# Performance work log

Measured on AMD Instinct MI355X. Metric: run time of the kernel, lower is better.

## Reference

```python
import jax, jax.numpy as jnp
import numpy as np
import math

K = 3            # max_rings
N_COMP = K + 2   # rings + center + background
RING_S = 0.02
BG_SIGMA = 0.94
CENTER_SIGMA = 0.01
NOISE_CAP = 0.15
COND_DIM, H_DIM = 64, 128
D_IN = COND_DIM + H_DIM


def setup_inputs() -> dict:
    key = jax.random.key(0)
    ks = jax.random.split(key, 12)
    sc = lambda fan_in: 1.0 / np.sqrt(fan_in)
    return {
        "c": jax.random.normal(ks[0], (1, COND_DIM), jnp.float32),
        "h": jax.random.normal(ks[1], (1, H_DIM), jnp.float32),
        # logits MLP: [D_IN, 128, 128, N_COMP]
        "W1": jax.random.normal(ks[2], (D_IN, 128), jnp.float32) * sc(D_IN),
        "b1": jnp.zeros((128,), jnp.float32),
        "W2": jax.random.normal(ks[3], (128, 128), jnp.float32) * sc(128),
        "b2": jnp.zeros((128,), jnp.float32),
        "W3": jax.random.normal(ks[4], (128, N_COMP), jnp.float32) * sc(128),
        "b3": jnp.zeros((N_COMP,), jnp.float32),
        # center_radius head: mus [K,2], Rs [K]
        "W_mu": jax.random.normal(ks[5], (D_IN, K * 2), jnp.float32) * sc(D_IN),
        "b_mu": jnp.zeros((K * 2,), jnp.float32),
        "W_R": jax.random.normal(ks[6], (D_IN, K), jnp.float32) * sc(D_IN),
        "b_R": jnp.ones((K,), jnp.float32) * 0.5,
        "N": 8388608,
    }


def _capped_weights(x, W1, b1, W2, b2, W3, b3):
    z = jax.nn.silu(x @ W1 + b1)
    z = jax.nn.silu(z @ W2 + b2)
    w = jax.nn.softmax(z @ W3 + b3, axis=-1)          # [1, N_COMP]
    w_bg = jnp.minimum(w[..., -1:], NOISE_CAP)
    w_rest = w[..., :-1]
    rest_sum = jnp.maximum(w_rest.sum(-1, keepdims=True), 1e-8)
    w_rest = w_rest * (1.0 - w_bg) / rest_sum
    return jnp.concatenate([w_rest, w_bg], axis=-1) + 1e-8


def reference(c, h, W1, b1, W2, b2, W3, b3, W_mu, b_mu, W_R, b_R, N):
    x = jnp.concatenate([c, h], axis=-1)              # [1, D_IN]
    w = _capped_weights(x, W1, b1, W2, b2, W3, b3)[0]  # [N_COMP]
    mus = (x @ W_mu + b_mu).reshape(K, 2)             # [K, 2]
    Rs = (x @ W_R + b_R)[0]                           # [K]

    key = jax.random.key(42)
    k_cat, k_th, k_r, k_eps = jax.random.split(key, 4)
    idx = jax.random.categorical(k_cat, jnp.log(w), shape=(N,))   # [N]
    jr = jnp.minimum(idx, K - 1)                      # safe ring index

    theta = jax.random.uniform(k_th, (N,), jnp.float32) * (2.0 * math.pi)
    r = Rs[jr] + RING_S * jax.random.normal(k_r, (N,), jnp.float32)
    ring_xy = jnp.stack([r * jnp.cos(theta), r * jnp.sin(theta)], axis=-1) + mus[jr]

    eps = jax.random.normal(k_eps, (N, 2), jnp.float32)
    center_xy = mus[0] + CENTER_SIGMA * eps
    bg_xy = mus[0] + BG_SIGMA * eps

    is_ring = (idx < K)[:, None]
    is_center = (idx == K)[:, None]
    xy = jnp.where(is_ring, ring_xy, jnp.where(is_center, center_xy, bg_xy))
    return xy, idx
```

## Files before the change

kernel.cpp:

```cpp
#include <hip/hip_runtime.h>
#include <math.h>

#define TFROT(v, r) (((v) << (r)) | ((v) >> (32 - (r))))

__device__ __forceinline__ void tf_block(unsigned k0, unsigned k1,
                                         unsigned x0, unsigned x1,
                                         unsigned &o0, unsigned &o1) {
  unsigned ks2 = k0 ^ k1 ^ 0x1BD11BDAu;
  x0 += k0; x1 += k1;
  x0 += x1; x1 = TFROT(x1, 13); x1 ^= x0;
  x0 += x1; x1 = TFROT(x1, 15); x1 ^= x0;
  x0 += x1; x1 = TFROT(x1, 26); x1 ^= x0;
  x0 += x1; x1 = TFROT(x1,  6); x1 ^= x0;
  x0 += k1; x1 += ks2 + 1u;
  x0 += x1; x1 = TFROT(x1, 17); x1 ^= x0;
  x0 += x1; x1 = TFROT(x1, 29); x1 ^= x0;
  x0 += x1; x1 = TFROT(x1, 16); x1 ^= x0;
  x0 += x1; x1 = TFROT(x1, 24); x1 ^= x0;
  x0 += ks2; x1 += k0 + 2u;
  x0 += x1; x1 = TFROT(x1, 13); x1 ^= x0;
  x0 += x1; x1 = TFROT(x1, 15); x1 ^= x0;
  x0 += x1; x1 = TFROT(x1, 26); x1 ^= x0;
  x0 += x1; x1 = TFROT(x1,  6); x1 ^= x0;
  x0 += k0; x1 += k1 + 3u;
  x0 += x1; x1 = TFROT(x1, 17); x1 ^= x0;
  x0 += x1; x1 = TFROT(x1, 29); x1 ^= x0;
  x0 += x1; x1 = TFROT(x1, 16); x1 ^= x0;
  x0 += x1; x1 = TFROT(x1, 24); x1 ^= x0;
  x0 += k1; x1 += ks2 + 4u;
  x0 += x1; x1 = TFROT(x1, 13); x1 ^= x0;
  x0 += x1; x1 = TFROT(x1, 15); x1 ^= x0;
  x0 += x1; x1 = TFROT(x1, 26); x1 ^= x0;
  x0 += x1; x1 = TFROT(x1,  6); x1 ^= x0;
  x0 += ks2; x1 += k0 + 5u;
  o0 = x0; o1 = x1;
}

__device__ __forceinline__ unsigned tf_bits32(unsigned k0, unsigned k1, unsigned i) {
  unsigned o0, o1;
  tf_block(k0, k1, 0u, i, o0, o1);
  return o0 ^ o1;
}

__device__ __forceinline__ float xla_exp_f32(float x) {
#pragma clang fp contract(off)
  const float kHi = 88.3762626647950f;
  const float kLo = -88.3762626647949f;
  const float kLog2e = 1.44269504088896341f;
  const float kC1 = 0.693359375f;
  const float kC2 = -2.12194440e-4f;
  const float p0 = 1.9875691500e-4f, p1 = 1.3981999507e-3f,
              p2 = 8.3334519073e-3f, p3 = 4.1665795894e-2f,
              p4 = 1.6666665459e-1f, p5 = 5.0000001201e-1f;
  float xc = fminf(fmaxf(x, kLo), kHi);
  float t = xc * kLog2e;
  t = t + 0.5f;
  float fx = floorf(t);
  float tmp = kC1 * fx;
  float z = kC2 * fx;
  float xr = xc - tmp;
  xr = xr - z;
  z = xr * xr;
  float y = p0 * xr;  y = y + p1;
  y = y * xr;  y = y + p2;
  y = y * xr;  y = y + p3;
  y = y * xr;  y = y + p4;
  y = y * xr;  y = y + p5;
  y = y * z;   y = y + xr;
  y = 1.0f + y;
  int emm0 = (int)fx;
  emm0 = (emm0 + 0x7f) << 23;
  float two_n = __int_as_float(emm0);
  float res = y * two_n;
  return fmaxf(res, x);
}

__device__ __forceinline__ float xla_log_f32(float x) {
#pragma clang fp contract(off)
  const float kSqrtHf = 0.707106781186547524f;
  const float p0 = 7.0376836292e-2f,  p1 = -1.1514610310e-1f,
              p2 = 1.1676998740e-1f,  p3 = -1.2420140846e-1f,
              p4 = 1.4249322787e-1f,  p5 = -1.6668057665e-1f,
              p6 = 2.0000714765e-1f,  p7 = -2.4999993993e-1f,
              p8 = 3.3333331174e-1f;
  const float q1 = -2.12194440e-4f, q2 = 0.693359375f;
  float t0 = fmaxf(x, __uint_as_float(0x00800000u));
  unsigned ib = __float_as_uint(t0);
  int ei = (int)(ib >> 23) - 0x7f;
  float e = (float)ei;
  e = e + 1.0f;
  t0 = __uint_as_float((ib & 0x807fffffu) | 0x3f000000u);
  bool m = (t0 < kSqrtHf);
  float tmp1 = m ? t0 : 0.0f;
  t0 = t0 - 1.0f;
  e = e - (m ? 1.0f : 0.0f);
  t0 = t0 + tmp1;
  float x2 = t0 * t0;
  float x3 = x2 * t0;
  float y, y1, y2;
  y  = p0 * t0;  y  = y  + p1;
  y1 = p3 * t0;  y1 = y1 + p4;
  y2 = p6 * t0;  y2 = y2 + p7;
  y  = y  * t0;  y  = y  + p2;
  y1 = y1 * t0;  y1 = y1 + p5;
  y2 = y2 * t0;  y2 = y2 + p8;
  y  = y * x3;   y  = y + y1;
  y  = y * x3;   y  = y + y2;
  y  = y * x3;
  y1 = e * q1;
  float tmp2 = x2 * 0.5f;
  y = y + y1;
  t0 = t0 - tmp2;
  y2 = e * q2;
  t0 = t0 + y;
  t0 = t0 + y2;
  return t0;
}

__device__ __forceinline__ float bits_to_f01(unsigned b) {
#pragma clang fp contract(off)
  return __uint_as_float((b >> 9) | 0x3f800000u) - 1.0f;
}

__device__ __forceinline__ float erfinv_f(float x) {
  float t = fmaf(-x, x, 1.0f);
  float w = -__logf(t);
  float p;
  if (w < 5.0f) {
    float v = w - 2.5f;
    p = 2.81022636e-08f;
    p = fmaf(p, v, 3.43273939e-07f);
    p = fmaf(p, v, -3.5233877e-06f);
    p = fmaf(p, v, -4.39150654e-06f);
    p = fmaf(p, v, 0.00021858087f);
    p = fmaf(p, v, -0.00125372503f);
    p = fmaf(p, v, -0.00417768164f);
    p = fmaf(p, v, 0.246640727f);
    p = fmaf(p, v, 1.50140941f);
  } else {
    float v = __fsqrt_rn(w) - 3.0f;
    p = -0.000200214257f;
    p = fmaf(p, v, 0.000100950558f);
    p = fmaf(p, v, 0.00134934322f);
    p = fmaf(p, v, -0.00367342844f);
    p = fmaf(p, v, 0.00573950773f);
    p = fmaf(p, v, -0.0076224613f);
    p = fmaf(p, v, 0.00943887047f);
    p = fmaf(p, v, 1.00167406f);
    p = fmaf(p, v, 2.83297682f);
  }
  return p * x;
}

struct Params {
  double mu[6];
  double Rs[3];
  float logits[5];
  unsigned keys[8];
};

__global__ void prep_kernel(const float* __restrict__ c, const float* __restrict__ h,
                            const float* __restrict__ W1, const float* __restrict__ b1,
                            const float* __restrict__ W2, const float* __restrict__ b2,
                            const float* __restrict__ W3, const float* __restrict__ b3,
                            const float* __restrict__ Wmu, const float* __restrict__ bmu,
                            const float* __restrict__ WR, const float* __restrict__ bR,
                            Params* __restrict__ P) {
#pragma clang fp contract(off)
  __shared__ float xs[192], z1[128], z2[128], z3[5];
  int t = threadIdx.x;
  if (t < 64) xs[t] = c[t];
  else if (t < 192) xs[t] = h[t - 64];
  __syncthreads();
  if (t < 128) {
    float acc = 0.0f;
    for (int k = 0; k < 192; ++k) { float pr = xs[k] * W1[k * 128 + t]; acc = acc + pr; }
    acc = acc + b1[t];
    float ex = xla_exp_f32(-acc);
    float den = 1.0f + ex;
    float sg = 1.0f / den;
    z1[t] = acc * sg;
  }
  __syncthreads();
  if (t < 128) {
    float acc = 0.0f;
    for (int k = 0; k < 128; ++k) { float pr = z1[k] * W2[k * 128 + t]; acc = acc + pr; }
    acc = acc + b2[t];
    float ex = xla_exp_f32(-acc);
    float den = 1.0f + ex;
    float sg = 1.0f / den;
    z2[t] = acc * sg;
  }
  __syncthreads();
  if (t < 5) {
    float acc = 0.0f;
    for (int k = 0; k < 128; ++k) { float pr = z2[k] * W3[k * 5 + t]; acc = acc + pr; }
    z3[t] = acc + b3[t];
  }
  if (t < 6) {
    double acc = 0.0;
    for (int k = 0; k < 192; ++k) acc += (double)xs[k] * (double)Wmu[k * 6 + t];
    P->mu[t] = acc + (double)bmu[t];
  }
  if (t < 3) {
    double acc = 0.0;
    for (int k = 0; k < 192; ++k) acc += (double)xs[k] * (double)WR[k * 3 + t];
    P->Rs[t] = acc + (double)bR[t];
  }
  __syncthreads();
  if (t == 0) {
    float mx = z3[0];
    for (int j = 1; j < 5; ++j) mx = fmaxf(mx, z3[j]);
    float ev[5];
    float ssum = 0.0f;
    for (int j = 0; j < 5; ++j) {
      float d = z3[j] - mx;
      ev[j] = xla_exp_f32(d);
      ssum = ssum + ev[j];
    }
    float w[5];
    for (int j = 0; j < 5; ++j) w[j] = ev[j] / ssum;
    float wbg = fminf(w[4], 0.15f);
    float rsum = 0.0f;
    for (int j = 0; j < 4; ++j) rsum = rsum + w[j];
    float rs = fmaxf(rsum, 1e-8f);
    float om = 1.0f - wbg;
    float wf[5];
    for (int j = 0; j < 4; ++j) {
      float a = w[j] * om;
      float bq = a / rs;
      wf[j] = bq + 1e-8f;
    }
    wf[4] = wbg + 1e-8f;
    for (int j = 0; j < 5; ++j) P->logits[j] = xla_log_f32(wf[j]);
    unsigned a0, a1;
    tf_block(0u, 42u, 0u, 0u, a0, a1); P->keys[0] = a0; P->keys[1] = a1;
    tf_block(0u, 42u, 0u, 1u, a0, a1); P->keys[2] = a0; P->keys[3] = a1;
    tf_block(0u, 42u, 0u, 2u, a0, a1); P->keys[4] = a0; P->keys[5] = a1;
    tf_block(0u, 42u, 0u, 3u, a0, a1); P->keys[6] = a0; P->keys[7] = a1;
  }
}

__global__ void __launch_bounds__(256)
sample_kernel(const Params* __restrict__ P, float* __restrict__ out, int N) {
#pragma clang fp contract(off)
  const float TINYF = __uint_as_float(0x00800000u);
  const float LOF   = __uint_as_float(0xBF7FFFFFu);
  const float TWOPIF = __uint_as_float(0x40C90FDBu);
  const float SQRT2F = 1.4142135623730951f;
  const float MARGIN = 1e-4f;

  float lg[5];
  float muf[6], Rsf[3];
  unsigned ky[8];
#pragma unroll
  for (int j = 0; j < 5; ++j) lg[j] = P->logits[j];
#pragma unroll
  for (int j = 0; j < 6; ++j) muf[j] = (float)P->mu[j];
#pragma unroll
  for (int j = 0; j < 3; ++j) Rsf[j] = (float)P->Rs[j];
#pragma unroll
  for (int j = 0; j < 8; ++j) ky[j] = P->keys[j];

  int T = gridDim.x * blockDim.x;
  for (int s = blockIdx.x * blockDim.x + threadIdx.x; s < N; s += T) {
    unsigned base = 5u * (unsigned)s;
    float uu[5];
    int bi = 0;
    float b1v = -__builtin_inff();
    float b2v = -__builtin_inff();
#pragma unroll
    for (int j = 0; j < 5; ++j) {
      unsigned b = tf_bits32(ky[0], ky[1], base + (unsigned)j);
      float u0 = bits_to_f01(b);
      float u = u0 + TINYF;
      u = fmaxf(TINYF, u);
      uu[j] = u;
      float l1 = __logf(u);
      float l2 = __logf(-l1);
      float sc = lg[j] - l2;
      bool gt = sc > b1v;
      float old1 = b1v;
      b1v = gt ? sc : b1v;
      b2v = gt ? old1 : fmaxf(b2v, sc);
      bi  = gt ? j : bi;
    }
    if (b1v - b2v < MARGIN) {
      int best = 0;
      float bestv = -__builtin_inff();
#pragma unroll
      for (int j = 0; j < 5; ++j) {
        float l1 = xla_log_f32(uu[j]);
        float nl1 = -l1;
        float l2 = xla_log_f32(nl1);
        float g = -l2;
        float sc = g + lg[j];
        if (sc > bestv) { bestv = sc; best = j; }
      }
      bi = best;
    }

    bool ring = bi < 3;
    unsigned cA = ring ? (unsigned)s : 2u * (unsigned)s;
    unsigned cB = ring ? (unsigned)s : 2u * (unsigned)s + 1u;
    unsigned kA0 = ring ? ky[2] : ky[6];
    unsigned kA1 = ring ? ky[3] : ky[7];
    unsigned kB0 = ring ? ky[4] : ky[6];
    unsigned kB1 = ring ? ky[5] : ky[7];
    unsigned bA = tf_bits32(kA0, kA1, cA);
    unsigned bB = tf_bits32(kB0, kB1, cB);

    float uB = fmaxf(LOF, fmaf(bits_to_f01(bB), 2.0f, LOF));
    float nB = SQRT2F * erfinv_f(uB);

    float ox, oy;
    if (ring) {
      float theta = bits_to_f01(bA) * TWOPIF;
      float r = fmaf(0.02f, nB, Rsf[bi]);
      ox = fmaf(r, __cosf(theta), muf[2 * bi + 0]);
      oy = fmaf(r, __sinf(theta), muf[2 * bi + 1]);
    } else {
      float uA = fmaxf(LOF, fmaf(bits_to_f01(bA), 2.0f, LOF));
      float nA = SQRT2F * erfinv_f(uA);
      float sg = (bi == 3) ? 0.01f : 0.94f;
      ox = fmaf(sg, nA, muf[0]);
      oy = fmaf(sg, nB, muf[1]);
    }

    reinterpret_cast<float2*>(out)[s] = make_float2(ox, oy);
    out[(size_t)2 * (size_t)N + (size_t)s] = (float)bi;
  }
}

extern "C" void kernel_launch(void* const* d_in, const int* in_sizes, int n_in,
                              void* d_out, int out_size, void* d_ws, size_t ws_size,
                              hipStream_t stream) {
  const float* c   = (const float*)d_in[0];
  const float* h   = (const float*)d_in[1];
  const float* W1  = (const float*)d_in[2];
  const float* b1  = (const float*)d_in[3];
  const float* W2  = (const float*)d_in[4];
  const float* b2  = (const float*)d_in[5];
  const float* W3  = (const float*)d_in[6];
  const float* b3  = (const float*)d_in[7];
  const float* Wmu = (const float*)d_in[8];
  const float* bmu = (const float*)d_in[9];
  const float* WR  = (const float*)d_in[10];
  const float* bR  = (const float*)d_in[11];
  (void)in_sizes; (void)n_in; (void)ws_size;

  int N = out_size / 3;
  Params* P = (Params*)d_ws;

  hipLaunchKernelGGL(prep_kernel, dim3(1), dim3(256), 0, stream,
                     c, h, W1, b1, W2, b2, W3, b3, Wmu, bmu, WR, bR, P);
  int blocks = 4096;
  hipLaunchKernelGGL(sample_kernel, dim3(blocks), dim3(256), 0, stream,
                     P, (float*)d_out, N);
}
```

Measured before the change: 205.0 us.

## Replace Gumbel argmax with exponential-race argmin and branchless output selection

Categorical sampling now uses an exponential race: it computes -log2(u)/w per component with precomputed inverse weights, so each of the five draws needs one log instead of two. A wider fallback test sends near-ties and extreme values to the exact XLA-log path. The ring/non-ring branches are replaced by computing both results and selecting, with hardware sin/cos taking the turns fraction directly, to avoid wavefront divergence. The trade-off is that every sample now does extra erfinv and sin/cos work, and the argmin may differ from the reference on near-ties that the fallback does not catch.

```diff
diff --git a/kernel.cpp b/kernel.cpp
--- a/kernel.cpp
+++ b/kernel.cpp
@@ -156,6 +156,7 @@
   double mu[6];
   double Rs[3];
   float logits[5];
+  float invw[5];
   unsigned keys[8];
 };
 
@@ -232,7 +233,10 @@
       wf[j] = bq + 1e-8f;
     }
     wf[4] = wbg + 1e-8f;
-    for (int j = 0; j < 5; ++j) P->logits[j] = xla_log_f32(wf[j]);
+    for (int j = 0; j < 5; ++j) {
+      P->logits[j] = xla_log_f32(wf[j]);
+      P->invw[j] = 1.0f / wf[j];
+    }
     unsigned a0, a1;
     tf_block(0u, 42u, 0u, 0u, a0, a1); P->keys[0] = a0; P->keys[1] = a1;
     tf_block(0u, 42u, 0u, 1u, a0, a1); P->keys[2] = a0; P->keys[3] = a1;
@@ -246,15 +250,15 @@
 #pragma clang fp contract(off)
   const float TINYF = __uint_as_float(0x00800000u);
   const float LOF   = __uint_as_float(0xBF7FFFFFu);
-  const float TWOPIF = __uint_as_float(0x40C90FDBu);
   const float SQRT2F = 1.4142135623730951f;
-  const float MARGIN = 1e-4f;
-
-  float lg[5];
+
+  float lg[5], cw[5];
   float muf[6], Rsf[3];
   unsigned ky[8];
 #pragma unroll
   for (int j = 0; j < 5; ++j) lg[j] = P->logits[j];
+#pragma unroll
+  for (int j = 0; j < 5; ++j) cw[j] = P->invw[j];
 #pragma unroll
   for (int j = 0; j < 6; ++j) muf[j] = (float)P->mu[j];
 #pragma unroll
@@ -265,32 +269,33 @@
   int T = gridDim.x * blockDim.x;
   for (int s = blockIdx.x * blockDim.x + threadIdx.x; s < N; s += T) {
     unsigned base = 5u * (unsigned)s;
-    float uu[5];
+    unsigned bb[5];
     int bi = 0;
-    float b1v = -__builtin_inff();
-    float b2v = -__builtin_inff();
+    float m1 = __builtin_inff();
+    float m2 = __builtin_inff();
 #pragma unroll
     for (int j = 0; j < 5; ++j) {
       unsigned b = tf_bits32(ky[0], ky[1], base + (unsigned)j);
+      bb[j] = b;
       float u0 = bits_to_f01(b);
-      float u = u0 + TINYF;
-      u = fmaxf(TINYF, u);
-      uu[j] = u;
-      float l1 = __logf(u);
-      float l2 = __logf(-l1);
-      float sc = lg[j] - l2;
-      bool gt = sc > b1v;
-      float old1 = b1v;
-      b1v = gt ? sc : b1v;
-      b2v = gt ? old1 : fmaxf(b2v, sc);
-      bi  = gt ? j : bi;
-    }
-    if (b1v - b2v < MARGIN) {
+      float e2 = -__log2f(u0);
+      float m = e2 * cw[j];
+      bool lt = m < m1;
+      float old1 = m1;
+      m1 = lt ? m : m1;
+      m2 = lt ? old1 : fminf(m2, m);
+      bi = lt ? j : bi;
+    }
+    bool slow = (m2 - m1 < 1e-3f * m2) || (m1 < 1e-4f) || (m2 > 1e37f);
+    if (slow) {
       int best = 0;
       float bestv = -__builtin_inff();
 #pragma unroll
       for (int j = 0; j < 5; ++j) {
-        float l1 = xla_log_f32(uu[j]);
+        float u0 = bits_to_f01(bb[j]);
+        float u = u0 + TINYF;
+        u = fmaxf(TINYF, u);
+        float l1 = xla_log_f32(u);
         float nl1 = -l1;
         float l2 = xla_log_f32(nl1);
         float g = -l2;
@@ -301,8 +306,9 @@
     }
 
     bool ring = bi < 3;
-    unsigned cA = ring ? (unsigned)s : 2u * (unsigned)s;
-    unsigned cB = ring ? (unsigned)s : 2u * (unsigned)s + 1u;
+    unsigned sU = (unsigned)s;
+    unsigned cA = ring ? sU : 2u * sU;
+    unsigned cB = ring ? sU : 2u * sU + 1u;
     unsigned kA0 = ring ? ky[2] : ky[6];
     unsigned kA1 = ring ? ky[3] : ky[7];
     unsigned kB0 = ring ? ky[4] : ky[6];
@@ -310,22 +316,26 @@
     unsigned bA = tf_bits32(kA0, kA1, cA);
     unsigned bB = tf_bits32(kB0, kB1, cB);
 
-    float uB = fmaxf(LOF, fmaf(bits_to_f01(bB), 2.0f, LOF));
+    float a01 = bits_to_f01(bA);
+    float b01 = bits_to_f01(bB);
+    float uB = fmaxf(LOF, fmaf(b01, 2.0f, LOF));
     float nB = SQRT2F * erfinv_f(uB);
 
-    float ox, oy;
-    if (ring) {
-      float theta = bits_to_f01(bA) * TWOPIF;
-      float r = fmaf(0.02f, nB, Rsf[bi]);
-      ox = fmaf(r, __cosf(theta), muf[2 * bi + 0]);
-      oy = fmaf(r, __sinf(theta), muf[2 * bi + 1]);
-    } else {
-      float uA = fmaxf(LOF, fmaf(bits_to_f01(bA), 2.0f, LOF));
-      float nA = SQRT2F * erfinv_f(uA);
-      float sg = (bi == 3) ? 0.01f : 0.94f;
-      ox = fmaf(sg, nA, muf[0]);
-      oy = fmaf(sg, nB, muf[1]);
-    }
+    float Rb = (bi == 0) ? Rsf[0] : ((bi == 1) ? Rsf[1] : Rsf[2]);
+    float mxr = (bi == 0) ? muf[0] : ((bi == 1) ? muf[2] : muf[4]);
+    float myr = (bi == 0) ? muf[1] : ((bi == 1) ? muf[3] : muf[5]);
+    float r = fmaf(0.02f, nB, Rb);
+    float rx = fmaf(r, __builtin_amdgcn_cosf(a01), mxr);
+    float ry = fmaf(r, __builtin_amdgcn_sinf(a01), myr);
+
+    float uA = fmaxf(LOF, fmaf(a01, 2.0f, LOF));
+    float nA = SQRT2F * erfinv_f(uA);
+    float sg = (bi == 3) ? 0.01f : 0.94f;
+    float ex = fmaf(sg, nA, muf[0]);
+    float ey = fmaf(sg, nB, muf[1]);
+
+    float ox = ring ? rx : ex;
+    float oy = ring ? ry : ey;
 
     reinterpret_cast<float2*>(out)[s] = make_float2(ox, oy);
     out[(size_t)2 * (size_t)N + (size_t)s] = (float)bi;
```

Result: faster. 193.8 us (-5.5%).
